# Optimization experiments

Hardware: AMD Instinct MI355X
Metric: run time of the kernel (lower is better)

The kernel has to match this reference:

```python
import jax, jax.numpy as jnp
import numpy as np

D_MODEL = 1024
NUM_HEADS = 16
DEPTH = D_MODEL // NUM_HEADS
MAX_LEN = 5000


def _make_pe(d_model=D_MODEL, max_len=MAX_LEN):
    # Faithful to torch PositionalEncoding: pe shape [max_len, 1, d_model]
    position = np.arange(max_len, dtype=np.float32)[:, None]
    div_term = np.exp(np.arange(0, d_model, 2, dtype=np.float32) * (-np.log(10000.0) / d_model))
    pe = np.zeros((max_len, d_model), dtype=np.float32)
    pe[:, 0::2] = np.sin(position * div_term)
    pe[:, 1::2] = np.cos(position * div_term)
    return jnp.asarray(pe[:, None, :])  # [max_len, 1, d_model]


def setup_inputs() -> dict:
    key = jax.random.key(0)
    ks = jax.random.split(key, 11)
    B, S, D = 4, 2048, D_MODEL
    s = 1.0 / np.sqrt(D)
    inp = {
        "v": jax.random.normal(ks[0], (B, S, D), jnp.float32),
        "k": jax.random.normal(ks[1], (B, S, D), jnp.float32),
        "q": jax.random.normal(ks[2], (B, S, D), jnp.float32),
        "wq_w": jax.random.normal(ks[3], (D, D), jnp.float32) * s,
        "wq_b": jnp.zeros((D,), jnp.float32),
        "wk_w": jax.random.normal(ks[4], (D, D), jnp.float32) * s,
        "wk_b": jnp.zeros((D,), jnp.float32),
        "wv_w": jax.random.normal(ks[5], (D, D), jnp.float32) * s,
        "wv_b": jnp.zeros((D,), jnp.float32),
        "dense_w": jax.random.normal(ks[6], (D, D), jnp.float32) * s,
        "dense_b": jnp.zeros((D,), jnp.float32),
        "pe": _make_pe(),
    }
    return inp


def _split_heads(x, B):
    # [B, S, D] -> [B, H, S, depth]
    return x.reshape(B, -1, NUM_HEADS, DEPTH).transpose(0, 2, 1, 3)


def reference(v, k, q, wq_w, wq_b, wk_w, wk_b, wv_w, wv_b, dense_w, dense_b, pe):
    B = q.shape[0]
    # Faithful bug-reproduction: pe[:batch] has shape [B, 1, D], broadcast over seq.
    pe_b = pe[:B]  # [B, 1, D]
    q = q + pe_b
    k = k + pe_b
    v = v + pe_b
    # Linear layers (torch: x @ W.T + b)
    qh = _split_heads(q @ wq_w.T + wq_b, B)  # [B,H,Sq,d]
    kh = _split_heads(k @ wk_w.T + wk_b, B)  # [B,H,Sk,d]
    vh = _split_heads(v @ wv_w.T + wv_b, B)  # [B,H,Sk,d]
    scale = 1.0 / jnp.sqrt(jnp.float32(DEPTH))
    logits = jnp.einsum("bhqd,bhkd->bhqk", qh, kh) * scale
    attn = jax.nn.softmax(logits, axis=-1)
    out = jnp.einsum("bhqk,bhkd->bhqd", attn, vh)
    out = out.transpose(0, 2, 1, 3).reshape(B, -1, D_MODEL)
    return out @ dense_w.T + dense_b
```

## Files before the change

### kernel.cpp

```cpp
#include <hip/hip_runtime.h>
#include <hip/hip_bf16.h>

typedef short short8 __attribute__((ext_vector_type(8)));
typedef float f32x4 __attribute__((ext_vector_type(4)));
typedef float f32x16 __attribute__((ext_vector_type(16)));
typedef unsigned int uint4v __attribute__((ext_vector_type(4)));

#define MFMA16(a, b, c) __builtin_amdgcn_mfma_f32_16x16x32_bf16(a, b, c, 0, 0, 0)
#define MFMA32(a, b, c) __builtin_amdgcn_mfma_f32_32x32x16_bf16(a, b, c, 0, 0, 0)

typedef __attribute__((address_space(1))) const unsigned int gas_u32;
typedef __attribute__((address_space(3))) unsigned int las_u32;

__device__ inline void gll16(const void* g, void* l) {
    __builtin_amdgcn_global_load_lds((gas_u32*)g, (las_u32*)l, 16, 0, 0);
}

__device__ inline unsigned short f2bf(float f) {
    unsigned u = __builtin_bit_cast(unsigned, f);
    u += 0x7fff + ((u >> 16) & 1);
    return (unsigned short)(u >> 16);
}

__device__ inline unsigned pk_perm(float a, float b, unsigned sel) {
    unsigned r;
    asm("v_perm_b32 %0, %1, %2, %3"
        : "=v"(r)
        : "v"(__builtin_bit_cast(unsigned, b)), "v"(__builtin_bit_cast(unsigned, a)), "s"(sel));
    return r;
}

__device__ inline float exp2_fast(float x) {
#if __has_builtin(__builtin_amdgcn_exp2f)
    return __builtin_amdgcn_exp2f(x);
#else
    float r; asm("v_exp_f32 %0, %1" : "=v"(r) : "v"(x)); return r;
#endif
}

__device__ inline void pl32_swap(unsigned &a, unsigned &b) {
    asm volatile("v_permlane32_swap_b32 %0, %1" : "+v"(a), "+v"(b));
}

__global__ void pe_cast3(const float* __restrict__ q, const float* __restrict__ k,
                         const float* __restrict__ v, const float* __restrict__ pe,
                         unsigned short* __restrict__ oq, unsigned short* __restrict__ ok,
                         unsigned short* __restrict__ ov) {
    const float* x = (blockIdx.y == 0) ? q : (blockIdx.y == 1) ? k : v;
    unsigned short* o = (blockIdx.y == 0) ? oq : (blockIdx.y == 1) ? ok : ov;
    int i = blockIdx.x * 256 + threadIdx.x;
    long e = (long)i * 4;
    int b = (int)(e >> 21);
    int d = (int)(e & 1023);
    float4 xv = reinterpret_cast<const float4*>(x)[i];
    float4 pv = *reinterpret_cast<const float4*>(pe + b * 1024 + d);
    ushort4 r;
    r.x = f2bf(xv.x + pv.x); r.y = f2bf(xv.y + pv.y);
    r.z = f2bf(xv.z + pv.z); r.w = f2bf(xv.w + pv.w);
    reinterpret_cast<ushort4*>(o)[i] = r;
}

__global__ void wcast4(const float* __restrict__ w0, const float* __restrict__ w1,
                       const float* __restrict__ w2, const float* __restrict__ w3,
                       unsigned short* __restrict__ o0) {
    const float* w = (blockIdx.y == 0) ? w0 : (blockIdx.y == 1) ? w1
                   : (blockIdx.y == 2) ? w2 : w3;
    unsigned short* o = o0 + (size_t)blockIdx.y * 1024 * 1024;
    int i = blockIdx.x * 256 + threadIdx.x;
    float4 xv = reinterpret_cast<const float4*>(w)[i];
    ushort4 r;
    r.x = f2bf(xv.x); r.y = f2bf(xv.y); r.z = f2bf(xv.z); r.w = f2bf(xv.w);
    reinterpret_cast<ushort4*>(o)[i] = r;
}

__global__ __launch_bounds__(512, 2) void gemm8(const unsigned short* __restrict__ A0,
                                                const unsigned short* __restrict__ W0,
                                                const float* __restrict__ bq,
                                                const float* __restrict__ bk,
                                                const float* __restrict__ bv,
                                                void* __restrict__ oq,
                                                void* __restrict__ ok,
                                                void* __restrict__ ov,
                                                float qscale) {
    const int NT = 16;
    __shared__ __align__(16) unsigned short lsA[2][256 * 64];
    __shared__ __align__(16) unsigned short lsB[2][256 * 64];

    int z = blockIdx.z;
    const unsigned short* A = A0 + (size_t)z * 8192 * 1024;
    const unsigned short* W = W0 + (size_t)z * 1024 * 1024;
    const float* bias = (z == 0) ? bq : (z == 1) ? bk : bv;
    float scale = (z == 0) ? qscale : 1.0f;

    int tid = threadIdx.x, wave = tid >> 6, lane = tid & 63;
    int lg = lane >> 4, l15 = lane & 15;
    int wr = wave >> 2, wc = wave & 3;
    int brow = blockIdx.x * 256;
    int bcol = blockIdx.y * 256;

    int srow = tid >> 3;
    int scol = ((tid ^ srow) & 7) * 8;
    const unsigned short* pA = A + (long)(brow + srow) * 1024 + scol;
    const unsigned short* pB = W + (long)(bcol + srow) * 1024 + scol;

    f32x4 acc[8][4];
#pragma unroll
    for (int m = 0; m < 8; ++m)
#pragma unroll
        for (int n = 0; n < 4; ++n) acc[m][n] = f32x4{0.f, 0.f, 0.f, 0.f};

#define SA(t, bi, q) gll16(pA + (t) * 64 + (q) * 65536,                     \
                           (char*)lsA[bi] + ((q) * 512 + wave * 64) * 16)
#define SB(t, bi, q) gll16(pB + (t) * 64 + (q) * 65536,                     \
                           (char*)lsB[bi] + ((q) * 512 + wave * 64) * 16)

    SB(0, 0, 0); SB(0, 0, 1); SB(0, 0, 2); SB(0, 0, 3);
    SA(0, 0, 0); SA(0, 0, 2); SA(0, 0, 1); SA(0, 0, 3);
    asm volatile("s_waitcnt vmcnt(2)" ::: "memory");
    __builtin_amdgcn_s_barrier();

    int swz_ = (l15 & 7) << 4;
    for (int t = 0; t < NT; ++t) {
        int cb = t & 1, nb = cb ^ 1;
        const char* KA = (const char*)lsA[cb];
        const char* KB = (const char*)lsB[cb];
        short8 af0[4][2], af1[4][2], bf0[2][2], bf1[2][2];
        const bool st = (t < NT - 1);

#pragma unroll
        for (int m = 0; m < 4; ++m)
#pragma unroll
            for (int kk = 0; kk < 2; ++kk)
                af0[m][kk] = *(const short8*)(KA + (wr * 128 + m * 16 + l15) * 128 +
                                              (((kk * 4 + lg) << 4) ^ swz_));
#pragma unroll
        for (int n = 0; n < 2; ++n)
#pragma unroll
            for (int kk = 0; kk < 2; ++kk)
                bf0[n][kk] = *(const short8*)(KB + (wc * 64 + n * 16 + l15) * 128 +
                                              (((kk * 4 + lg) << 4) ^ swz_));
        if (st) { SB(t + 1, nb, 0); SB(t + 1, nb, 1); }
        __builtin_amdgcn_s_barrier();
        asm volatile("s_waitcnt lgkmcnt(0)" ::: "memory");
        __builtin_amdgcn_s_setprio(1);
#pragma unroll
        for (int m = 0; m < 4; ++m)
#pragma unroll
            for (int n = 0; n < 2; ++n)
#pragma unroll
                for (int kk = 0; kk < 2; ++kk)
                    acc[m][n] = MFMA16(af0[m][kk], bf0[n][kk], acc[m][n]);
        __builtin_amdgcn_s_setprio(0);
        __builtin_amdgcn_s_barrier();

#pragma unroll
        for (int n = 0; n < 2; ++n)
#pragma unroll
            for (int kk = 0; kk < 2; ++kk)
                bf1[n][kk] = *(const short8*)(KB + (wc * 64 + (n + 2) * 16 + l15) * 128 +
                                              (((kk * 4 + lg) << 4) ^ swz_));
        if (st) { SB(t + 1, nb, 2); SB(t + 1, nb, 3); }
        if (st) { asm volatile("s_waitcnt vmcnt(4)" ::: "memory"); }
        else    { asm volatile("s_waitcnt vmcnt(0)" ::: "memory"); }
        __builtin_amdgcn_s_barrier();
        asm volatile("s_waitcnt lgkmcnt(0)" ::: "memory");
        __builtin_amdgcn_s_setprio(1);
#pragma unroll
        for (int m = 0; m < 4; ++m)
#pragma unroll
            for (int n = 0; n < 2; ++n)
#pragma unroll
                for (int kk = 0; kk < 2; ++kk)
                    acc[m][n + 2] = MFMA16(af0[m][kk], bf1[n][kk], acc[m][n + 2]);
        __builtin_amdgcn_s_setprio(0);
        __builtin_amdgcn_s_barrier();

#pragma unroll
        for (int m = 0; m < 4; ++m)
#pragma unroll
            for (int kk = 0; kk < 2; ++kk)
                af1[m][kk] = *(const short8*)(KA + (wr * 128 + (m + 4) * 16 + l15) * 128 +
                                              (((kk * 4 + lg) << 4) ^ swz_));
        if (st) { SA(t + 1, nb, 0); SA(t + 1, nb, 2); }
        __builtin_amdgcn_s_barrier();
        asm volatile("s_waitcnt lgkmcnt(0)" ::: "memory");
        __builtin_amdgcn_s_setprio(1);
#pragma unroll
        for (int m = 0; m < 4; ++m)
#pragma unroll
            for (int n = 0; n < 2; ++n)
#pragma unroll
                for (int kk = 0; kk < 2; ++kk)
                    acc[m + 4][n] = MFMA16(af1[m][kk], bf0[n][kk], acc[m + 4][n]);
        __builtin_amdgcn_s_setprio(0);
        __builtin_amdgcn_s_barrier();

        if (st) {
            SA(t + 1, nb, 1); SA(t + 1, nb, 3);
            asm volatile("s_waitcnt vmcnt(2)" ::: "memory");
        }
        __builtin_amdgcn_s_barrier();
        __builtin_amdgcn_s_setprio(1);
#pragma unroll
        for (int m = 0; m < 4; ++m)
#pragma unroll
            for (int n = 0; n < 2; ++n)
#pragma unroll
                for (int kk = 0; kk < 2; ++kk)
                    acc[m + 4][n + 2] = MFMA16(af1[m][kk], bf1[n][kk], acc[m + 4][n + 2]);
        __builtin_amdgcn_s_setprio(0);
        __builtin_amdgcn_s_barrier();
    }
#undef SA
#undef SB

    void* out = (z == 0) ? oq : (z == 1) ? ok : ov;
#pragma unroll
    for (int m = 0; m < 8; ++m)
#pragma unroll
        for (int n = 0; n < 4; ++n) {
            int col = bcol + wc * 64 + n * 16 + l15;
            float bv_ = bias[col];
            int row0 = brow + wr * 128 + m * 16 + lg * 4;
            if (z == 2) {
                int b = row0 >> 11, s0 = row0 & 2047;
                ushort4 pk;
                pk.x = f2bf(acc[m][n][0] + bv_);
                pk.y = f2bf(acc[m][n][1] + bv_);
                pk.z = f2bf(acc[m][n][2] + bv_);
                pk.w = f2bf(acc[m][n][3] + bv_);
                *(ushort4*)((unsigned short*)out + ((long)(b * 1024 + col)) * 2048 + s0) = pk;
            } else {
#pragma unroll
                for (int r = 0; r < 4; ++r) {
                    int row = row0 + r;
                    float v = (acc[m][n][r] + bv_) * scale;
                    int b = row >> 11, s = row & 2047, h = col >> 6, d = col & 63;
                    ((unsigned short*)out)[(((long)(b * 16 + h) * 2048 + s) * 64 + d)] = f2bf(v);
                }
            }
        }
}

__global__ __launch_bounds__(256, 3) void gemm_dense(const unsigned short* __restrict__ A,
                                                     const unsigned short* __restrict__ W,
                                                     const float* __restrict__ bias,
                                                     float* __restrict__ out) {
    const int NT = 32;
    __shared__ unsigned short lsA[3][128 * 32];
    __shared__ unsigned short lsB[3][128 * 32];

    int flat = blockIdx.x;
    int xcd = flat & 7;
    int s = flat >> 3;
    int brow = (xcd * 8 + (s & 7)) * 128;
    int bcol = (s >> 3) * 128;

    int tid = threadIdx.x;
    int wave = tid >> 6, lane = tid & 63, lg = lane >> 4, l15 = lane & 15;
    int wr = wave >> 1, wc = wave & 1;

    int c0 = wave * 64 + lane, c1 = 256 + c0;
    const unsigned short* sA0 = A + (long)(brow + (c0 >> 2)) * 1024 + ((c0 ^ (c0 >> 2)) & 3) * 8;
    const unsigned short* sA1 = A + (long)(brow + (c1 >> 2)) * 1024 + ((c1 ^ (c1 >> 2)) & 3) * 8;
    const unsigned short* sB0 = W + (long)(bcol + (c0 >> 2)) * 1024 + ((c0 ^ (c0 >> 2)) & 3) * 8;
    const unsigned short* sB1 = W + (long)(bcol + (c1 >> 2)) * 1024 + ((c1 ^ (c1 >> 2)) & 3) * 8;

    int cread = (lg * 16) ^ ((l15 & 3) << 4);

    f32x4 acc[4][4];
#pragma unroll
    for (int m = 0; m < 4; ++m)
#pragma unroll
        for (int n = 0; n < 4; ++n) acc[m][n] = f32x4{0.f, 0.f, 0.f, 0.f};

#define STG(k0, bi) do {                                                  \
        gll16(sA0 + (k0), (char*)lsA[bi] + (wave * 64) * 16);             \
        gll16(sA1 + (k0), (char*)lsA[bi] + (256 + wave * 64) * 16);       \
        gll16(sB0 + (k0), (char*)lsB[bi] + (wave * 64) * 16);             \
        gll16(sB1 + (k0), (char*)lsB[bi] + (256 + wave * 64) * 16);       \
    } while (0)

    STG(0, 0);
    STG(32, 1);

    int bi = 0, sb = 2;
    for (int t = 0; t < NT; ++t) {
        if (t == NT - 1) { asm volatile("s_waitcnt vmcnt(0)" ::: "memory"); }
        else             { asm volatile("s_waitcnt vmcnt(4)" ::: "memory"); }
        __builtin_amdgcn_s_barrier();
        if (t < NT - 2) STG((t + 2) * 32, sb);

        const char* KA = (const char*)lsA[bi];
        const char* KB = (const char*)lsB[bi];
        short8 af[4], bf_[4];
#pragma unroll
        for (int m = 0; m < 4; ++m) {
            int row = wr * 64 + m * 16 + l15;
            af[m] = *(const short8*)(KA + row * 64 + cread);
        }
#pragma unroll
        for (int n = 0; n < 4; ++n) {
            int col = wc * 64 + n * 16 + l15;
            bf_[n] = *(const short8*)(KB + col * 64 + cread);
        }
        __builtin_amdgcn_s_setprio(1);
#pragma unroll
        for (int m = 0; m < 4; ++m)
#pragma unroll
            for (int n = 0; n < 4; ++n) acc[m][n] = MFMA16(af[m], bf_[n], acc[m][n]);
        __builtin_amdgcn_s_setprio(0);

        bi = (bi == 2) ? 0 : bi + 1;
        sb = (sb == 2) ? 0 : sb + 1;
    }
#undef STG

#pragma unroll
    for (int m = 0; m < 4; ++m)
#pragma unroll
        for (int n = 0; n < 4; ++n) {
            int col = bcol + wc * 64 + n * 16 + l15;
            float bv_ = bias[col];
#pragma unroll
            for (int r = 0; r < 4; ++r) {
                int row = brow + wr * 64 + m * 16 + lg * 4 + r;
                out[(long)row * 1024 + col] = acc[m][n][r] + bv_;
            }
        }
}

__global__ __launch_bounds__(256, 2) void attn_kernel(const unsigned short* __restrict__ Qh,
                                                      const unsigned short* __restrict__ Kh,
                                                      const unsigned short* __restrict__ Vt,
                                                      unsigned short* __restrict__ Om) {
    const int S = 2048;
    const int NT = S / 64;
    int flat = blockIdx.x;
    int nf_ = (flat & 7) * 64 + (flat >> 3);
    int qt = nf_ & 7;
    int bh = nf_ >> 3;
    int b = bh >> 4, h = bh & 15;

    int tid = threadIdx.x, wave = tid >> 6, lane = tid & 63;
    int l31 = lane & 31, hi = lane >> 5;

    __shared__ __align__(16) unsigned short Kl[3][4096];
    __shared__ __align__(16) unsigned short Vtl[3][4096];

    const unsigned short* Qb = Qh + (long)bh * S * 64;
    const unsigned short* Kb = Kh + (long)bh * S * 64;
    const unsigned short* Vb = Vt + (long)bh * 64 * S;

    int colS = ((((tid & 7) * 16) ^ (((tid >> 3) & 7) << 4)) >> 1);
    const unsigned short* srcK = Kb + (tid >> 3) * 64 + colS;
    const unsigned short* srcV = Vb + (tid >> 3) * 2048 + colS;

    short8 aq[2][4];
    {
        const unsigned short* qrow = Qb + (long)(qt * 256 + wave * 64 + l31) * 64 + hi * 8;
#pragma unroll
        for (int qf = 0; qf < 2; ++qf)
#pragma unroll
            for (int s = 0; s < 4; ++s)
                aq[qf][s] = *(const short8*)(qrow + qf * 32 * 64 + s * 16);
    }

    f32x16 oacc[2][2], lacc[2], z16;
#pragma unroll
    for (int r = 0; r < 16; ++r) {
        oacc[0][0][r] = 0.f; oacc[0][1][r] = 0.f;
        oacc[1][0][r] = 0.f; oacc[1][1][r] = 0.f;
        lacc[0][r] = 0.f; lacc[1][r] = 0.f;
        z16[r] = 0.f;
    }

    const short8 ones8 = {0x3F80, 0x3F80, 0x3F80, 0x3F80, 0x3F80, 0x3F80, 0x3F80, 0x3F80};
    const unsigned SEL = 0x07060302u;

    int rb0 = l31 * 128;
    int swz = (l31 & 7) << 4;

#define STAGE(kt, bi) do {                                              \
        const unsigned short* sk = srcK + (kt) * 4096;                  \
        gll16(sk,         (char*)Kl[bi] + wave * 1024);                 \
        gll16(sk + 2048,  (char*)Kl[bi] + 4096 + wave * 1024);          \
        const unsigned short* sv = srcV + (kt) * 64;                    \
        gll16(sv,         (char*)Vtl[bi] + wave * 1024);                \
        gll16(sv + 65536, (char*)Vtl[bi] + 4096 + wave * 1024);         \
    } while (0)

    STAGE(0, 0);
    STAGE(1, 1);

    int bi = 0, sb = 2;
    for (int kt = 0; kt < NT; ++kt) {
        if (kt == NT - 1) { asm volatile("s_waitcnt vmcnt(0)" ::: "memory"); }
        else              { asm volatile("s_waitcnt vmcnt(4)" ::: "memory"); }
        __builtin_amdgcn_s_barrier();
        if (kt < NT - 2) STAGE(kt + 2, sb);

        const char* KlC = (const char*)Kl[bi];
        const char* VlC = (const char*)Vtl[bi];

        f32x16 sacc[2][2];
        __builtin_amdgcn_s_setprio(1);
#pragma unroll
        for (int blk = 0; blk < 2; ++blk) {
            short8 kf0 = *(const short8*)(KlC + blk * 4096 + rb0 + ((16 * hi) ^ swz));
            sacc[0][blk] = MFMA32(kf0, aq[0][0], z16);
            sacc[1][blk] = MFMA32(kf0, aq[1][0], z16);
#pragma unroll
            for (int s = 1; s < 4; ++s) {
                short8 kf = *(const short8*)(KlC + blk * 4096 + rb0 + ((32 * s + 16 * hi) ^ swz));
                sacc[0][blk] = MFMA32(kf, aq[0][s], sacc[0][blk]);
                sacc[1][blk] = MFMA32(kf, aq[1][s], sacc[1][blk]);
            }
        }
        __builtin_amdgcn_s_setprio(0);

#pragma unroll
        for (int qf = 0; qf < 2; ++qf)
#pragma unroll
            for (int blk = 0; blk < 2; ++blk)
#pragma unroll
                for (int r = 0; r < 16; ++r) sacc[qf][blk][r] = exp2_fast(sacc[qf][blk][r]);

#pragma unroll
        for (int s = 0; s < 4; ++s) {
            const int blk = s >> 1, base = (s & 1) * 8;
            short8 pa[2];
#pragma unroll
            for (int qf = 0; qf < 2; ++qf) {
                unsigned q0 = pk_perm(sacc[qf][blk][base + 0], sacc[qf][blk][base + 1], SEL);
                unsigned q1 = pk_perm(sacc[qf][blk][base + 2], sacc[qf][blk][base + 3], SEL);
                unsigned q2 = pk_perm(sacc[qf][blk][base + 4], sacc[qf][blk][base + 5], SEL);
                unsigned q3 = pk_perm(sacc[qf][blk][base + 6], sacc[qf][blk][base + 7], SEL);
                pl32_swap(q0, q2);
                pl32_swap(q1, q3);
                uint4v pw; pw[0] = q0; pw[1] = q1; pw[2] = q2; pw[3] = q3;
                pa[qf] = __builtin_bit_cast(short8, pw);
            }
            __builtin_amdgcn_s_setprio(1);
#pragma unroll
            for (int dblk = 0; dblk < 2; ++dblk) {
                short8 vf = *(const short8*)(VlC + dblk * 4096 + rb0 + ((32 * s + 16 * hi) ^ swz));
                oacc[0][dblk] = MFMA32(pa[0], vf, oacc[0][dblk]);
                oacc[1][dblk] = MFMA32(pa[1], vf, oacc[1][dblk]);
            }
            lacc[0] = MFMA32(pa[0], ones8, lacc[0]);
            lacc[1] = MFMA32(pa[1], ones8, lacc[1]);
            __builtin_amdgcn_s_setprio(0);
        }
        bi = (bi == 2) ? 0 : bi + 1;
        sb = (sb == 2) ? 0 : sb + 1;
    }
#undef STAGE

#pragma unroll
    for (int qf = 0; qf < 2; ++qf) {
        float inv[16];
#pragma unroll
        for (int r = 0; r < 16; ++r) inv[r] = 1.0f / lacc[qf][r];
        int qrow0 = qt * 256 + wave * 64 + qf * 32 + 4 * hi;
#pragma unroll
        for (int dblk = 0; dblk < 2; ++dblk)
#pragma unroll
            for (int r = 0; r < 16; ++r) {
                int qrow = qrow0 + (r & 3) + 8 * (r >> 2);
                int d = h * 64 + dblk * 32 + l31;
                float v = oacc[qf][dblk][r] * inv[r];
                Om[((long)b * 2048 + qrow) * 1024 + d] = f2bf(v);
            }
    }
}

extern "C" void kernel_launch(void* const* d_in, const int* in_sizes, int n_in,
                              void* d_out, int out_size, void* d_ws, size_t ws_size,
                              hipStream_t stream) {
    const float* v_in = (const float*)d_in[0];
    const float* k_in = (const float*)d_in[1];
    const float* q_in = (const float*)d_in[2];
    const float* wq_w = (const float*)d_in[3];
    const float* wq_b = (const float*)d_in[4];
    const float* wk_w = (const float*)d_in[5];
    const float* wk_b = (const float*)d_in[6];
    const float* wv_w = (const float*)d_in[7];
    const float* wv_b = (const float*)d_in[8];
    const float* wd_w = (const float*)d_in[9];
    const float* wd_b = (const float*)d_in[10];
    const float* pe   = (const float*)d_in[11];

    const long SZ = 8192L * 1024 * 2;
    char* ws = (char*)d_ws;
    unsigned short* xq = (unsigned short*)(ws + 0);
    unsigned short* xk = (unsigned short*)(ws + SZ);
    unsigned short* xv = (unsigned short*)(ws + 2 * SZ);
    unsigned short* qh = (unsigned short*)(ws + 3 * SZ);
    unsigned short* kh = (unsigned short*)(ws + 4 * SZ);
    unsigned short* vt = (unsigned short*)(ws + 5 * SZ);
    unsigned short* wqb16 = (unsigned short*)(ws + 6 * SZ);

    pe_cast3<<<dim3(8192, 3), 256, 0, stream>>>(q_in, k_in, v_in, pe, xq, xk, xv);
    wcast4<<<dim3(1024, 4), 256, 0, stream>>>(wq_w, wk_w, wv_w, wd_w, wqb16);

    const float QSCALE = 0.125f * 1.44269504088896f;
    gemm8<<<dim3(32, 4, 3), 512, 0, stream>>>(
        xq, wqb16, wq_b, wk_b, wv_b, qh, kh, vt, QSCALE);

    unsigned short* om = xq;
    attn_kernel<<<512, 256, 0, stream>>>(qh, kh, vt, om);

    gemm_dense<<<512, 256, 0, stream>>>(
        om, wqb16 + 3L * 1024 * 1024, wd_b, (float*)d_out);
}
```

Baseline: 205.5 us.

## Persist QKV projection blocks: each does one Q/K tile plus half a V tile

Replaces the 3D grid of 384 equal tiles with 256 blocks that each compute one 256x256 Q or K tile and then a 256x128 slice of the V projection. This balances work across CUs and avoids the partial-wave tail of the old grid. The V phase uses a simpler double-buffered loop with a different wave layout, which may overlap loads less well than the main path.

```diff
diff --git a/kernel.cpp b/kernel.cpp
--- a/kernel.cpp
+++ b/kernel.cpp
@@ -73,173 +73,249 @@
     reinterpret_cast<ushort4*>(o)[i] = r;
 }
 
-__global__ __launch_bounds__(512, 2) void gemm8(const unsigned short* __restrict__ A0,
-                                                const unsigned short* __restrict__ W0,
-                                                const float* __restrict__ bq,
-                                                const float* __restrict__ bk,
-                                                const float* __restrict__ bv,
-                                                void* __restrict__ oq,
-                                                void* __restrict__ ok,
-                                                void* __restrict__ ov,
-                                                float qscale) {
+__global__ __launch_bounds__(512, 2) void gemm8p(const unsigned short* __restrict__ A0,
+                                                 const unsigned short* __restrict__ W0,
+                                                 const float* __restrict__ bq,
+                                                 const float* __restrict__ bk,
+                                                 const float* __restrict__ bv,
+                                                 unsigned short* __restrict__ oq,
+                                                 unsigned short* __restrict__ ok,
+                                                 unsigned short* __restrict__ ov,
+                                                 float qscale) {
     const int NT = 16;
     __shared__ __align__(16) unsigned short lsA[2][256 * 64];
     __shared__ __align__(16) unsigned short lsB[2][256 * 64];
 
-    int z = blockIdx.z;
-    const unsigned short* A = A0 + (size_t)z * 8192 * 1024;
-    const unsigned short* W = W0 + (size_t)z * 1024 * 1024;
-    const float* bias = (z == 0) ? bq : (z == 1) ? bk : bv;
-    float scale = (z == 0) ? qscale : 1.0f;
-
+    int blk = blockIdx.x;
     int tid = threadIdx.x, wave = tid >> 6, lane = tid & 63;
     int lg = lane >> 4, l15 = lane & 15;
-    int wr = wave >> 2, wc = wave & 3;
-    int brow = blockIdx.x * 256;
-    int bcol = blockIdx.y * 256;
-
     int srow = tid >> 3;
     int scol = ((tid ^ srow) & 7) * 8;
-    const unsigned short* pA = A + (long)(brow + srow) * 1024 + scol;
-    const unsigned short* pB = W + (long)(bcol + srow) * 1024 + scol;
-
-    f32x4 acc[8][4];
-#pragma unroll
-    for (int m = 0; m < 8; ++m)
-#pragma unroll
-        for (int n = 0; n < 4; ++n) acc[m][n] = f32x4{0.f, 0.f, 0.f, 0.f};
+    int swz_ = (l15 & 7) << 4;
+
+    {
+        int z = blk >> 7;
+        int rem = blk & 127;
+        int brow = (rem >> 2) * 256;
+        int bcol = (rem & 3) * 256;
+        const unsigned short* A = A0 + (size_t)z * 8192 * 1024;
+        const unsigned short* W = W0 + (size_t)z * 1024 * 1024;
+        const float* bias = (z == 0) ? bq : bk;
+        float scale = (z == 0) ? qscale : 1.0f;
+        unsigned short* out = (z == 0) ? oq : ok;
+
+        int wr = wave >> 2, wc = wave & 3;
+        const unsigned short* pA = A + (long)(brow + srow) * 1024 + scol;
+        const unsigned short* pB = W + (long)(bcol + srow) * 1024 + scol;
+
+        f32x4 acc[8][4];
+#pragma unroll
+        for (int m = 0; m < 8; ++m)
+#pragma unroll
+            for (int n = 0; n < 4; ++n) acc[m][n] = f32x4{0.f, 0.f, 0.f, 0.f};
 
 #define SA(t, bi, q) gll16(pA + (t) * 64 + (q) * 65536,                     \
                            (char*)lsA[bi] + ((q) * 512 + wave * 64) * 16)
 #define SB(t, bi, q) gll16(pB + (t) * 64 + (q) * 65536,                     \
                            (char*)lsB[bi] + ((q) * 512 + wave * 64) * 16)
 
-    SB(0, 0, 0); SB(0, 0, 1); SB(0, 0, 2); SB(0, 0, 3);
-    SA(0, 0, 0); SA(0, 0, 2); SA(0, 0, 1); SA(0, 0, 3);
-    asm volatile("s_waitcnt vmcnt(2)" ::: "memory");
-    __builtin_amdgcn_s_barrier();
-
-    int swz_ = (l15 & 7) << 4;
-    for (int t = 0; t < NT; ++t) {
-        int cb = t & 1, nb = cb ^ 1;
-        const char* KA = (const char*)lsA[cb];
-        const char* KB = (const char*)lsB[cb];
-        short8 af0[4][2], af1[4][2], bf0[2][2], bf1[2][2];
-        const bool st = (t < NT - 1);
-
-#pragma unroll
-        for (int m = 0; m < 4; ++m)
-#pragma unroll
-            for (int kk = 0; kk < 2; ++kk)
-                af0[m][kk] = *(const short8*)(KA + (wr * 128 + m * 16 + l15) * 128 +
-                                              (((kk * 4 + lg) << 4) ^ swz_));
-#pragma unroll
-        for (int n = 0; n < 2; ++n)
-#pragma unroll
-            for (int kk = 0; kk < 2; ++kk)
-                bf0[n][kk] = *(const short8*)(KB + (wc * 64 + n * 16 + l15) * 128 +
-                                              (((kk * 4 + lg) << 4) ^ swz_));
-        if (st) { SB(t + 1, nb, 0); SB(t + 1, nb, 1); }
+        SB(0, 0, 0); SB(0, 0, 1); SB(0, 0, 2); SB(0, 0, 3);
+        SA(0, 0, 0); SA(0, 0, 2); SA(0, 0, 1); SA(0, 0, 3);
+        asm volatile("s_waitcnt vmcnt(2)" ::: "memory");
         __builtin_amdgcn_s_barrier();
-        asm volatile("s_waitcnt lgkmcnt(0)" ::: "memory");
-        __builtin_amdgcn_s_setprio(1);
-#pragma unroll
-        for (int m = 0; m < 4; ++m)
+
+        for (int t = 0; t < NT; ++t) {
+            int cb = t & 1, nb = cb ^ 1;
+            const char* KA = (const char*)lsA[cb];
+            const char* KB = (const char*)lsB[cb];
+            short8 af0[4][2], af1[4][2], bf0[2][2], bf1[2][2];
+            const bool st = (t < NT - 1);
+
+#pragma unroll
+            for (int m = 0; m < 4; ++m)
+#pragma unroll
+                for (int kk = 0; kk < 2; ++kk)
+                    af0[m][kk] = *(const short8*)(KA + (wr * 128 + m * 16 + l15) * 128 +
+                                                  (((kk * 4 + lg) << 4) ^ swz_));
 #pragma unroll
             for (int n = 0; n < 2; ++n)
 #pragma unroll
                 for (int kk = 0; kk < 2; ++kk)
-                    acc[m][n] = MFMA16(af0[m][kk], bf0[n][kk], acc[m][n]);
-        __builtin_amdgcn_s_setprio(0);
-        __builtin_amdgcn_s_barrier();
-
-#pragma unroll
-        for (int n = 0; n < 2; ++n)
-#pragma unroll
-            for (int kk = 0; kk < 2; ++kk)
-                bf1[n][kk] = *(const short8*)(KB + (wc * 64 + (n + 2) * 16 + l15) * 128 +
-                                              (((kk * 4 + lg) << 4) ^ swz_));
-        if (st) { SB(t + 1, nb, 2); SB(t + 1, nb, 3); }
-        if (st) { asm volatile("s_waitcnt vmcnt(4)" ::: "memory"); }
-        else    { asm volatile("s_waitcnt vmcnt(0)" ::: "memory"); }
-        __builtin_amdgcn_s_barrier();
-        asm volatile("s_waitcnt lgkmcnt(0)" ::: "memory");
-        __builtin_amdgcn_s_setprio(1);
-#pragma unroll
-        for (int m = 0; m < 4; ++m)
+                    bf0[n][kk] = *(const short8*)(KB + (wc * 64 + n * 16 + l15) * 128 +
+                                                  (((kk * 4 + lg) << 4) ^ swz_));
+            if (st) { SB(t + 1, nb, 0); SB(t + 1, nb, 1); }
+            __builtin_amdgcn_s_barrier();
+            asm volatile("s_waitcnt lgkmcnt(0)" ::: "memory");
+            __builtin_amdgcn_s_setprio(1);
+#pragma unroll
+            for (int m = 0; m < 4; ++m)
+#pragma unroll
+                for (int n = 0; n < 2; ++n)
+#pragma unroll
+                    for (int kk = 0; kk < 2; ++kk)
+                        acc[m][n] = MFMA16(af0[m][kk], bf0[n][kk], acc[m][n]);
+            __builtin_amdgcn_s_setprio(0);
+            __builtin_amdgcn_s_barrier();
+
 #pragma unroll
             for (int n = 0; n < 2; ++n)
 #pragma unroll
                 for (int kk = 0; kk < 2; ++kk)
-                    acc[m][n + 2] = MFMA16(af0[m][kk], bf1[n][kk], acc[m][n + 2]);
-        __builtin_amdgcn_s_setprio(0);
-        __builtin_amdgcn_s_barrier();
-
-#pragma unroll
-        for (int m = 0; m < 4; ++m)
-#pragma unroll
-            for (int kk = 0; kk < 2; ++kk)
-                af1[m][kk] = *(const short8*)(KA + (wr * 128 + (m + 4) * 16 + l15) * 128 +
-                                              (((kk * 4 + lg) << 4) ^ swz_));
-        if (st) { SA(t + 1, nb, 0); SA(t + 1, nb, 2); }
-        __builtin_amdgcn_s_barrier();
-        asm volatile("s_waitcnt lgkmcnt(0)" ::: "memory");
-        __builtin_amdgcn_s_setprio(1);
-#pragma unroll
-        for (int m = 0; m < 4; ++m)
-#pragma unroll
-            for (int n = 0; n < 2; ++n)
+                    bf1[n][kk] = *(const short8*)(KB + (wc * 64 + (n + 2) * 16 + l15) * 128 +
+                                                  (((kk * 4 + lg) << 4) ^ swz_));
+            if (st) { SB(t + 1, nb, 2); SB(t + 1, nb, 3); }
+            if (st) { asm volatile("s_waitcnt vmcnt(4)" ::: "memory"); }
+            else    { asm volatile("s_waitcnt vmcnt(0)" ::: "memory"); }
+            __builtin_amdgcn_s_barrier();
+            asm volatile("s_waitcnt lgkmcnt(0)" ::: "memory");
+            __builtin_amdgcn_s_setprio(1);
+#pragma unroll
+            for (int m = 0; m < 4; ++m)
+#pragma unroll
+                for (int n = 0; n < 2; ++n)
+#pragma unroll
+                    for (int kk = 0; kk < 2; ++kk)
+                        acc[m][n + 2] = MFMA16(af0[m][kk], bf1[n][kk], acc[m][n + 2]);
+            __builtin_amdgcn_s_setprio(0);
+            __builtin_amdgcn_s_barrier();
+
+#pragma unroll
+            for (int m = 0; m < 4; ++m)
 #pragma unroll
                 for (int kk = 0; kk < 2; ++kk)
-                    acc[m + 4][n] = MFMA16(af1[m][kk], bf0[n][kk], acc[m + 4][n]);
-        __builtin_amdgcn_s_setprio(0);
-        __builtin_amdgcn_s_barrier();
-
-        if (st) {
-            SA(t + 1, nb, 1); SA(t + 1, nb, 3);
-            asm volatile("s_waitcnt vmcnt(2)" ::: "memory");
-        }
-        __builtin_amdgcn_s_barrier();
-        __builtin_amdgcn_s_setprio(1);
-#pragma unroll
-        for (int m = 0; m < 4; ++m)
-#pragma unroll
-            for (int n = 0; n < 2; ++n)
-#pragma unroll
-                for (int kk = 0; kk < 2; ++kk)
-                    acc[m + 4][n + 2] = MFMA16(af1[m][kk], bf1[n][kk], acc[m + 4][n + 2]);
-        __builtin_amdgcn_s_setprio(0);
-        __builtin_amdgcn_s_barrier();
-    }
+                    af1[m][kk] = *(const short8*)(KA + (wr * 128 + (m + 4) * 16 + l15) * 128 +
+                                                  (((kk * 4 + lg) << 4) ^ swz_));
+            if (st) { SA(t + 1, nb, 0); SA(t + 1, nb, 2); }
+            __builtin_amdgcn_s_barrier();
+            asm volatile("s_waitcnt lgkmcnt(0)" ::: "memory");
+            __builtin_amdgcn_s_setprio(1);
+#pragma unroll
+            for (int m = 0; m < 4; ++m)
+#pragma unroll
+                for (int n = 0; n < 2; ++n)
+#pragma unroll
+                    for (int kk = 0; kk < 2; ++kk)
+                        acc[m + 4][n] = MFMA16(af1[m][kk], bf0[n][kk], acc[m + 4][n]);
+            __builtin_amdgcn_s_setprio(0);
+            __builtin_amdgcn_s_barrier();
+
+            if (st) {
+                SA(t + 1, nb, 1); SA(t + 1, nb, 3);
+                asm volatile("s_waitcnt vmcnt(2)" ::: "memory");
+            }
+            __builtin_amdgcn_s_barrier();
+            __builtin_amdgcn_s_setprio(1);
+#pragma unroll
+            for (int m = 0; m < 4; ++m)
+#pragma unroll
+                for (int n = 0; n < 2; ++n)
+#pragma unroll
+                    for (int kk = 0; kk < 2; ++kk)
+                        acc[m + 4][n + 2] = MFMA16(af1[m][kk], bf1[n][kk], acc[m + 4][n + 2]);
+            __builtin_amdgcn_s_setprio(0);
+            __builtin_amdgcn_s_barrier();
+        }
 #undef SA
 #undef SB
 
-    void* out = (z == 0) ? oq : (z == 1) ? ok : ov;
-#pragma unroll
-    for (int m = 0; m < 8; ++m)
-#pragma unroll
-        for (int n = 0; n < 4; ++n) {
-            int col = bcol + wc * 64 + n * 16 + l15;
-            float bv_ = bias[col];
-            int row0 = brow + wr * 128 + m * 16 + lg * 4;
-            if (z == 2) {
+#pragma unroll
+        for (int m = 0; m < 8; ++m)
+#pragma unroll
+            for (int n = 0; n < 4; ++n) {
+                int col = bcol + wc * 64 + n * 16 + l15;
+                float bv_ = bias[col];
+                int row0 = brow + wr * 128 + m * 16 + lg * 4;
+#pragma unroll
+                for (int r = 0; r < 4; ++r) {
+                    int row = row0 + r;
+                    float v = (acc[m][n][r] + bv_) * scale;
+                    int b = row >> 11, s = row & 2047, h = col >> 6, d = col & 63;
+                    out[(((long)(b * 16 + h) * 2048 + s) * 64 + d)] = f2bf(v);
+                }
+            }
+    }
+
+    {
+        int ti = blk >> 1;
+        int brow = (ti >> 2) * 256;
+        int bcol = (ti & 3) * 256 + (blk & 1) * 128;
+        const unsigned short* A = A0 + (size_t)2 * 8192 * 1024;
+        const unsigned short* W = W0 + (size_t)2 * 1024 * 1024;
+
+        int wr = wave >> 1, wc = wave & 1;
+        const unsigned short* pA = A + (long)(brow + srow) * 1024 + scol;
+        const unsigned short* pB = W + (long)(bcol + srow) * 1024 + scol;
+
+        f32x4 acc[4][4];
+#pragma unroll
+        for (int m = 0; m < 4; ++m)
+#pragma unroll
+            for (int n = 0; n < 4; ++n) acc[m][n] = f32x4{0.f, 0.f, 0.f, 0.f};
+
+#define SA2(t, bi, q) gll16(pA + (t) * 64 + (q) * 65536,                     \
+                            (char*)lsA[bi] + ((q) * 512 + wave * 64) * 16)
+#define SB2(t, bi, q) gll16(pB + (t) * 64 + (q) * 65536,                     \
+                            (char*)lsB[bi] + ((q) * 512 + wave * 64) * 16)
+
+        SB2(0, 0, 0); SB2(0, 0, 1);
+        SA2(0, 0, 0); SA2(0, 0, 1); SA2(0, 0, 2); SA2(0, 0, 3);
+
+        for (int t = 0; t < NT; ++t) {
+            int cb = t & 1, nb = cb ^ 1;
+            if (t < NT - 1) {
+                SB2(t + 1, nb, 0); SB2(t + 1, nb, 1);
+                SA2(t + 1, nb, 0); SA2(t + 1, nb, 1); SA2(t + 1, nb, 2); SA2(t + 1, nb, 3);
+                asm volatile("s_waitcnt vmcnt(6)" ::: "memory");
+            } else {
+                asm volatile("s_waitcnt vmcnt(0)" ::: "memory");
+            }
+            __builtin_amdgcn_s_barrier();
+
+            const char* KA = (const char*)lsA[cb];
+            const char* KB = (const char*)lsB[cb];
+            short8 af[4][2], bf[4][2];
+#pragma unroll
+            for (int m = 0; m < 4; ++m)
+#pragma unroll
+                for (int kk = 0; kk < 2; ++kk)
+                    af[m][kk] = *(const short8*)(KA + (wr * 64 + m * 16 + l15) * 128 +
+                                                 (((kk * 4 + lg) << 4) ^ swz_));
+#pragma unroll
+            for (int n = 0; n < 4; ++n)
+#pragma unroll
+                for (int kk = 0; kk < 2; ++kk)
+                    bf[n][kk] = *(const short8*)(KB + (wc * 64 + n * 16 + l15) * 128 +
+                                                 (((kk * 4 + lg) << 4) ^ swz_));
+            __builtin_amdgcn_s_setprio(1);
+#pragma unroll
+            for (int m = 0; m < 4; ++m)
+#pragma unroll
+                for (int n = 0; n < 4; ++n)
+#pragma unroll
+                    for (int kk = 0; kk < 2; ++kk)
+                        acc[m][n] = MFMA16(af[m][kk], bf[n][kk], acc[m][n]);
+            __builtin_amdgcn_s_setprio(0);
+            __builtin_amdgcn_s_barrier();
+        }
+#undef SA2
+#undef SB2
+
+#pragma unroll
+        for (int m = 0; m < 4; ++m)
+#pragma unroll
+            for (int n = 0; n < 4; ++n) {
+                int col = bcol + wc * 64 + n * 16 + l15;
+                float bv_ = bv[col];
+                int row0 = brow + wr * 64 + m * 16 + lg * 4;
                 int b = row0 >> 11, s0 = row0 & 2047;
                 ushort4 pk;
                 pk.x = f2bf(acc[m][n][0] + bv_);
                 pk.y = f2bf(acc[m][n][1] + bv_);
                 pk.z = f2bf(acc[m][n][2] + bv_);
                 pk.w = f2bf(acc[m][n][3] + bv_);
-                *(ushort4*)((unsigned short*)out + ((long)(b * 1024 + col)) * 2048 + s0) = pk;
-            } else {
-#pragma unroll
-                for (int r = 0; r < 4; ++r) {
-                    int row = row0 + r;
-                    float v = (acc[m][n][r] + bv_) * scale;
-                    int b = row >> 11, s = row & 2047, h = col >> 6, d = col & 63;
-                    ((unsigned short*)out)[(((long)(b * 16 + h) * 2048 + s) * 64 + d)] = f2bf(v);
-                }
-            }
-        }
+                *(ushort4*)(ov + ((long)(b * 1024 + col)) * 2048 + s0) = pk;
+            }
+    }
 }
 
 __global__ __launch_bounds__(256, 3) void gemm_dense(const unsigned short* __restrict__ A,
@@ -505,7 +581,7 @@
     wcast4<<<dim3(1024, 4), 256, 0, stream>>>(wq_w, wk_w, wv_w, wd_w, wqb16);
 
     const float QSCALE = 0.125f * 1.44269504088896f;
-    gemm8<<<dim3(32, 4, 3), 512, 0, stream>>>(
+    gemm8p<<<256, 512, 0, stream>>>(
         xq, wqb16, wq_b, wk_b, wv_b, qh, kh, vt, QSCALE);
 
     unsigned short* om = xq;
```

Result: no change. 203.3 us (-1.1%).
